# Performance work log

Measured on AMD Instinct MI355X. Metric: run time of the kernel, lower is better.

The kernel has to match this reference:

```python
import jax, jax.numpy as jnp
import numpy as np

NEG_SLOPE = 0.01  # torch nn.LeakyReLU default
K = 16

def lrelu(x):
    return jax.nn.leaky_relu(x, NEG_SLOPE)

def _knn_idx(src, dst, batch_src, batch_dst, k):
    # For each dst node, k nearest src nodes (euclidean, within same graph).
    # [Nd, Ns] squared distances; mask cross-graph pairs with +inf.
    d2 = (jnp.sum(dst * dst, axis=1)[:, None]
          + jnp.sum(src * src, axis=1)[None, :]
          - 2.0 * dst @ src.T)
    d2 = jnp.where(batch_dst[:, None] != batch_src[None, :], jnp.inf, d2)
    _, idx = jax.lax.top_k(-d2, k)  # [Nd, k] indices into src
    return idx

def _dynamic_edge_conv(src, dst, batch_src, batch_dst, w, b, k=K):
    # PyG DynamicEdgeConv: edge_index = knn(src, dst); message = nn([x_i, x_j - x_i]); max-aggregate.
    idx = _knn_idx(src, dst, batch_src, batch_dst, k)
    x_j = src[idx]                      # [Nd, k, D] gathered neighbors
    x_i = dst[:, None, :]               # [Nd, 1, D] center (target) features
    e = jnp.concatenate([jnp.broadcast_to(x_i, x_j.shape), x_j - x_i], axis=-1)  # [Nd, k, 2D]
    h = lrelu(e @ w + b)                # edge MLP: Linear(2D, D) + LeakyReLU
    return jnp.max(h, axis=1)           # max aggregation over k neighbors

def _mlp2(x, w1, b1, w2, b2):
    return lrelu(lrelu(x @ w1 + b1) @ w2 + b2)

def setup_inputs() -> dict:
    key = jax.random.key(0)
    ks = jax.random.split(key, 20)
    N_PFC, N_VTX, G, H = 8192, 2048, 32, 32
    def w(k, shp):
        return 0.1 * jax.random.normal(k, shp, jnp.float32)
    z = lambda n: jnp.zeros((n,), jnp.float32)
    return {
        "x_pfc": jax.random.normal(ks[0], (N_PFC, 7), jnp.float32),
        "x_vtx": jax.random.normal(ks[1], (N_VTX, 4), jnp.float32),
        "batch_pfc": jnp.sort(jax.random.randint(ks[2], (N_PFC,), 0, G)),
        "batch_vtx": jnp.sort(jax.random.randint(ks[3], (N_VTX,), 0, G)),
        "pfc_w1": w(ks[4], (7, H)),  "pfc_b1": z(H),
        "pfc_w2": w(ks[5], (H, H)),  "pfc_b2": z(H),
        "vtx_w1": w(ks[6], (4, H)),  "vtx_b1": z(H),
        "vtx_w2": w(ks[7], (H, H)),  "vtx_b2": z(H),
        "conv_w": w(ks[8], (2 * H, H)), "conv_b": z(H),
        "out_w1": w(ks[9], (H, 64)),  "out_b1": z(64),
        "out_w2": w(ks[10], (64, 32)), "out_b2": z(32),
        "out_w3": w(ks[11], (32, 4)),  "out_b3": z(4),
        "out_w4": w(ks[12], (4, 1)),   "out_b4": z(1),
    }

def reference(x_pfc, x_vtx, batch_pfc, batch_vtx,
              pfc_w1, pfc_b1, pfc_w2, pfc_b2,
              vtx_w1, vtx_b1, vtx_w2, vtx_b2,
              conv_w, conv_b,
              out_w1, out_b1, out_w2, out_b2, out_w3, out_b3, out_w4, out_b4):
    x_pfc_enc = _mlp2(x_pfc, pfc_w1, pfc_b1, pfc_w2, pfc_b2)   # [Npfc, 32]
    x_vtx_enc = _mlp2(x_vtx, vtx_w1, vtx_b1, vtx_w2, vtx_b2)   # [Nvtx, 32]
    # conv 1: pfc -> pfc (self knn)
    feats1 = _dynamic_edge_conv(x_pfc_enc, x_pfc_enc, batch_pfc, batch_pfc, conv_w, conv_b)
    # conv 2: vtx -> pfc (bipartite knn), same shared edge-MLP weights
    feats2 = _dynamic_edge_conv(x_vtx_enc, feats1, batch_vtx, batch_pfc, conv_w, conv_b)
    h = lrelu(feats2 @ out_w1 + out_b1)
    h = lrelu(h @ out_w2 + out_b2)
    h = lrelu(h @ out_w3 + out_b3)
    out = lrelu(h @ out_w4 + out_b4)    # [Npfc, 1]
    return (out, batch_pfc)
```

## Files before the change

### kernel.cpp

```cpp
#include <hip/hip_runtime.h>
#include <hip/hip_bf16.h>

#define LRELU(val) ((val) >= 0.0f ? (val) : 0.01f * (val))

__device__ __forceinline__ float dot4(float4 a, float4 b, float acc) {
    return fmaf(a.x, b.x, fmaf(a.y, b.y, fmaf(a.z, b.z, fmaf(a.w, b.w, acc))));
}

__device__ __forceinline__ float wdot4(const float* __restrict__ wbase, int c, int q,
                                       float4 a, float acc) {
    acc = fmaf(a.x, wbase[(4 * q + 0) * 32 + c], acc);
    acc = fmaf(a.y, wbase[(4 * q + 1) * 32 + c], acc);
    acc = fmaf(a.z, wbase[(4 * q + 2) * 32 + c], acc);
    acc = fmaf(a.w, wbase[(4 * q + 3) * 32 + c], acc);
    return acc;
}

__device__ inline int lower_bound_i(const int* __restrict__ a, int n, int v) {
    int lo = 0, hi = n;
    while (lo < hi) {
        int m = (lo + hi) >> 1;
        if (a[m] < v) lo = m + 1; else hi = m;
    }
    return lo;
}

__device__ __forceinline__ unsigned slot_key(
    int s, int lane, int start, int len, int Ns,
    const float* __restrict__ srcf, const float* __restrict__ srcn, float ni,
    float4 x0, float4 x1, float4 x2, float4 x3,
    float4 x4, float4 x5, float4 x6, float4 x7)
{
    const int o = lane + 64 * s;
    const bool valid = o < len;
    const int j = valid ? (start + o) : min(start, Ns - 1);
    const float4* rr = reinterpret_cast<const float4*>(srcf + (size_t)j * 32);
    float dot = 0.0f;
    dot = dot4(rr[0], x0, dot); dot = dot4(rr[1], x1, dot);
    dot = dot4(rr[2], x2, dot); dot = dot4(rr[3], x3, dot);
    dot = dot4(rr[4], x4, dot); dot = dot4(rr[5], x5, dot);
    dot = dot4(rr[6], x6, dot); dot = dot4(rr[7], x7, dot);
    float d2 = (ni + srcn[j]) - 2.0f * dot;
    unsigned u = __float_as_uint(d2);
    u = (d2 < 0.0f) ? ~u : (u | 0x80000000u);
    return valid ? u : 0xFFFFFFFFu;
}

template <int NSL>
__device__ __forceinline__ void select_compact(
    unsigned k0, unsigned k1, unsigned k2, unsigned k3, unsigned k4, unsigned k5,
    unsigned T, int start, int Ns, int* __restrict__ widxW, int lane)
{
    const unsigned long long below = (1ull << lane) - 1ull;
    int m = __popcll(__ballot(k0 < T));
    if (NSL > 1) m += __popcll(__ballot(k1 < T));
    if (NSL > 2) m += __popcll(__ballot(k2 < T));
    if (NSL > 3) m += __popcll(__ballot(k3 < T));
    if (NSL > 4) m += __popcll(__ballot(k4 < T));
    if (NSL > 5) m += __popcll(__ballot(k5 < T));
    const int need = 16 - m;
    const unsigned long long e0 = __ballot(k0 == T);
    const unsigned long long e1 = (NSL > 1) ? __ballot(k1 == T) : 0ull;
    const unsigned long long e2 = (NSL > 2) ? __ballot(k2 == T) : 0ull;
    const unsigned long long e3 = (NSL > 3) ? __ballot(k3 == T) : 0ull;
    const unsigned long long e4 = (NSL > 4) ? __ballot(k4 == T) : 0ull;
    const int eq0 = __popcll(e0), eq1 = eq0 + __popcll(e1), eq2 = eq1 + __popcll(e2),
              eq3 = eq2 + __popcll(e3), eq4 = eq3 + __popcll(e4);
    const bool sel0 = (k0 < T) || ((k0 == T) && (__popcll(e0 & below) < need));
    const bool sel1 = (NSL > 1) && ((k1 < T) || ((k1 == T) && (eq0 + __popcll(e1 & below) < need)));
    const bool sel2 = (NSL > 2) && ((k2 < T) || ((k2 == T) && (eq1 + __popcll(e2 & below) < need)));
    const bool sel3 = (NSL > 3) && ((k3 < T) || ((k3 == T) && (eq2 + __popcll(e3 & below) < need)));
    const bool sel4 = (NSL > 4) && ((k4 < T) || ((k4 == T) && (eq3 + __popcll(e4 & below) < need)));
    const bool sel5 = (NSL > 5) && ((k5 < T) || ((k5 == T) && (eq4 + __popcll(__ballot(k5 == T) & below) < need)));
    const unsigned long long s0 = __ballot(sel0);
    const unsigned long long s1 = __ballot(sel1);
    const unsigned long long s2 = __ballot(sel2);
    const unsigned long long s3 = __ballot(sel3);
    const unsigned long long s4 = __ballot(sel4);
    const unsigned long long s5 = __ballot(sel5);
    const int c0 = __popcll(s0), c1 = c0 + __popcll(s1), c2 = c1 + __popcll(s2),
              c3 = c2 + __popcll(s3), c4 = c3 + __popcll(s4);
    if (lane < 16) widxW[lane] = min(start, Ns - 1);
    __builtin_amdgcn_wave_barrier();
    if (sel0) widxW[__popcll(s0 & below)] = start + lane;
    if (NSL > 1 && sel1) widxW[c0 + __popcll(s1 & below)] = start + lane + 64;
    if (NSL > 2 && sel2) widxW[c1 + __popcll(s2 & below)] = start + lane + 128;
    if (NSL > 3 && sel3) widxW[c2 + __popcll(s3 & below)] = start + lane + 192;
    if (NSL > 4 && sel4) widxW[c3 + __popcll(s4 & below)] = start + lane + 256;
    if (NSL > 5 && sel5) widxW[c4 + __popcll(s5 & below)] = start + lane + 320;
    __builtin_amdgcn_wave_barrier();
}

template <int NSL>
__device__ __forceinline__ void conv_pair(
    float4 ax0, float4 ax1, float4 ax2, float4 ax3,
    float4 ax4, float4 ax5, float4 ax6, float4 ax7,
    float niA, int startA, int lenA,
    float4 bx0, float4 bx1, float4 bx2, float4 bx3,
    float4 bx4, float4 bx5, float4 bx6, float4 bx7,
    float niB, int startB, int lenB,
    const float* __restrict__ srcf, const float* __restrict__ srcn, int Ns,
    const float* __restrict__ W, const float* __restrict__ Bc,
    float4 w20, float4 w21, float4 w22, float4 w23,
    float4 w24, float4 w25, float4 w26, float4 w27,
    float4* __restrict__ sNbrA, float4* __restrict__ sNbrB,
    int* __restrict__ widxA, int* __restrict__ widxB,
    int lane, float& vOutA, float& vOutB)
{
    unsigned kA0 = 0xFFFFFFFFu, kA1 = 0xFFFFFFFFu, kA2 = 0xFFFFFFFFu,
             kA3 = 0xFFFFFFFFu, kA4 = 0xFFFFFFFFu, kA5 = 0xFFFFFFFFu;
    unsigned kB0 = 0xFFFFFFFFu, kB1 = 0xFFFFFFFFu, kB2 = 0xFFFFFFFFu,
             kB3 = 0xFFFFFFFFu, kB4 = 0xFFFFFFFFu, kB5 = 0xFFFFFFFFu;
    kA0 = slot_key(0, lane, startA, lenA, Ns, srcf, srcn, niA, ax0, ax1, ax2, ax3, ax4, ax5, ax6, ax7);
    kB0 = slot_key(0, lane, startB, lenB, Ns, srcf, srcn, niB, bx0, bx1, bx2, bx3, bx4, bx5, bx6, bx7);
    if (NSL > 1) {
        if (lenA > 64)  kA1 = slot_key(1, lane, startA, lenA, Ns, srcf, srcn, niA, ax0, ax1, ax2, ax3, ax4, ax5, ax6, ax7);
        if (lenB > 64)  kB1 = slot_key(1, lane, startB, lenB, Ns, srcf, srcn, niB, bx0, bx1, bx2, bx3, bx4, bx5, bx6, bx7);
    }
    if (NSL > 2) {
        if (lenA > 128) kA2 = slot_key(2, lane, startA, lenA, Ns, srcf, srcn, niA, ax0, ax1, ax2, ax3, ax4, ax5, ax6, ax7);
        if (lenB > 128) kB2 = slot_key(2, lane, startB, lenB, Ns, srcf, srcn, niB, bx0, bx1, bx2, bx3, bx4, bx5, bx6, bx7);
    }
    if (NSL > 3) {
        if (lenA > 192) kA3 = slot_key(3, lane, startA, lenA, Ns, srcf, srcn, niA, ax0, ax1, ax2, ax3, ax4, ax5, ax6, ax7);
        if (lenB > 192) kB3 = slot_key(3, lane, startB, lenB, Ns, srcf, srcn, niB, bx0, bx1, bx2, bx3, bx4, bx5, bx6, bx7);
    }
    if (NSL > 4) {
        if (lenA > 256) kA4 = slot_key(4, lane, startA, lenA, Ns, srcf, srcn, niA, ax0, ax1, ax2, ax3, ax4, ax5, ax6, ax7);
        if (lenB > 256) kB4 = slot_key(4, lane, startB, lenB, Ns, srcf, srcn, niB, bx0, bx1, bx2, bx3, bx4, bx5, bx6, bx7);
    }
    if (NSL > 5) {
        if (lenA > 320) kA5 = slot_key(5, lane, startA, lenA, Ns, srcf, srcn, niA, ax0, ax1, ax2, ax3, ax4, ax5, ax6, ax7);
        if (lenB > 320) kB5 = slot_key(5, lane, startB, lenB, Ns, srcf, srcn, niB, bx0, bx1, bx2, bx3, bx4, bx5, bx6, bx7);
    }

    unsigned loA = 0u, hiA = 0xFFFFFFFFu, loB = 0u, hiB = 0xFFFFFFFFu;
#pragma unroll 1
    for (int it = 0; it < 32; ++it) {
        const unsigned mA = loA + ((hiA - loA) >> 1);
        const unsigned mB = loB + ((hiB - loB) >> 1);
        int cA = __popcll(__ballot(kA0 <= mA));
        int cB = __popcll(__ballot(kB0 <= mB));
        if (NSL > 1) { cA += __popcll(__ballot(kA1 <= mA)); cB += __popcll(__ballot(kB1 <= mB)); }
        if (NSL > 2) { cA += __popcll(__ballot(kA2 <= mA)); cB += __popcll(__ballot(kB2 <= mB)); }
        if (NSL > 3) { cA += __popcll(__ballot(kA3 <= mA)); cB += __popcll(__ballot(kB3 <= mB)); }
        if (NSL > 4) { cA += __popcll(__ballot(kA4 <= mA)); cB += __popcll(__ballot(kB4 <= mB)); }
        if (NSL > 5) { cA += __popcll(__ballot(kA5 <= mA)); cB += __popcll(__ballot(kB5 <= mB)); }
        if (loA != hiA) { if (cA >= 16) hiA = mA; else loA = mA + 1; }
        if (loB != hiB) { if (cB >= 16) hiB = mB; else loB = mB + 1; }
        if (loA == hiA && loB == hiB) break;
    }

    select_compact<NSL>(kA0, kA1, kA2, kA3, kA4, kA5, loA, startA, Ns, widxA, lane);
    select_compact<NSL>(kB0, kB1, kB2, kB3, kB4, kB5, loB, startB, Ns, widxB, lane);

    const int c = lane & 31;
    const int n0 = lane >> 3, qq = lane & 7;
    const int n1 = n0 + 8;
    int jA0 = widxA[n0]; jA0 = ((unsigned)jA0 < (unsigned)Ns) ? jA0 : 0;
    int jA1 = widxA[n1]; jA1 = ((unsigned)jA1 < (unsigned)Ns) ? jA1 : 0;
    int jB0 = widxB[n0]; jB0 = ((unsigned)jB0 < (unsigned)Ns) ? jB0 : 0;
    int jB1 = widxB[n1]; jB1 = ((unsigned)jB1 < (unsigned)Ns) ? jB1 : 0;
    const float4* S = reinterpret_cast<const float4*>(srcf);
    const float4 rA0 = S[(size_t)jA0 * 8 + qq];
    const float4 rA1 = S[(size_t)jA1 * 8 + qq];
    const float4 rB0 = S[(size_t)jB0 * 8 + qq];
    const float4 rB1 = S[(size_t)jB1 * 8 + qq];

    float baseA = Bc[c];
    baseA = wdot4(W, c, 0, ax0, baseA); baseA = wdot4(W, c, 1, ax1, baseA);
    baseA = wdot4(W, c, 2, ax2, baseA); baseA = wdot4(W, c, 3, ax3, baseA);
    baseA = wdot4(W, c, 4, ax4, baseA); baseA = wdot4(W, c, 5, ax5, baseA);
    baseA = wdot4(W, c, 6, ax6, baseA); baseA = wdot4(W, c, 7, ax7, baseA);
    float dA = 0.0f;
    dA = dot4(ax0, w20, dA); dA = dot4(ax1, w21, dA); dA = dot4(ax2, w22, dA); dA = dot4(ax3, w23, dA);
    dA = dot4(ax4, w24, dA); dA = dot4(ax5, w25, dA); dA = dot4(ax6, w26, dA); dA = dot4(ax7, w27, dA);
    const float cbaseA = baseA - dA;

    float baseB = Bc[c];
    baseB = wdot4(W, c, 0, bx0, baseB); baseB = wdot4(W, c, 1, bx1, baseB);
    baseB = wdot4(W, c, 2, bx2, baseB); baseB = wdot4(W, c, 3, bx3, baseB);
    baseB = wdot4(W, c, 4, bx4, baseB); baseB = wdot4(W, c, 5, bx5, baseB);
    baseB = wdot4(W, c, 6, bx6, baseB); baseB = wdot4(W, c, 7, bx7, baseB);
    float dB = 0.0f;
    dB = dot4(bx0, w20, dB); dB = dot4(bx1, w21, dB); dB = dot4(bx2, w22, dB); dB = dot4(bx3, w23, dB);
    dB = dot4(bx4, w24, dB); dB = dot4(bx5, w25, dB); dB = dot4(bx6, w26, dB); dB = dot4(bx7, w27, dB);
    const float cbaseB = baseB - dB;

    sNbrA[n0 * 8 + qq] = rA0;
    sNbrA[n1 * 8 + qq] = rA1;
    sNbrB[n0 * 8 + qq] = rB0;
    sNbrB[n1 * 8 + qq] = rB1;
    __builtin_amdgcn_wave_barrier();

    const int half = lane >> 5;
    float vmA = -__builtin_huge_valf(), vmB = -__builtin_huge_valf();
#pragma unroll 1
    for (int r = 0; r < 8; ++r) {
        const float4* nA = sNbrA + (2 * r + half) * 8;
        const float4* nB = sNbrB + (2 * r + half) * 8;
        float accA = cbaseA, accB = cbaseB;
        accA = dot4(nA[0], w20, accA); accB = dot4(nB[0], w20, accB);
        accA = dot4(nA[1], w21, accA); accB = dot4(nB[1], w21, accB);
        accA = dot4(nA[2], w22, accA); accB = dot4(nB[2], w22, accB);
        accA = dot4(nA[3], w23, accA); accB = dot4(nB[3], w23, accB);
        accA = dot4(nA[4], w24, accA); accB = dot4(nB[4], w24, accB);
        accA = dot4(nA[5], w25, accA); accB = dot4(nB[5], w25, accB);
        accA = dot4(nA[6], w26, accA); accB = dot4(nB[6], w26, accB);
        accA = dot4(nA[7], w27, accA); accB = dot4(nB[7], w27, accB);
        vmA = fmaxf(vmA, LRELU(accA));
        vmB = fmaxf(vmB, LRELU(accB));
    }
    vmA = fmaxf(vmA, __shfl_xor(vmA, 32));
    vmB = fmaxf(vmB, __shfl_xor(vmB, 32));
    vOutA = vmA;
    vOutB = vmB;
}

__launch_bounds__(256)
__global__ void encode_kernel(const float* __restrict__ x_pfc, const float* __restrict__ x_vtx,
                              const int* __restrict__ bpfc, const int* __restrict__ bvtx,
                              const float* __restrict__ pw1, const float* __restrict__ pb1,
                              const float* __restrict__ pw2, const float* __restrict__ pb2,
                              const float* __restrict__ vw1, const float* __restrict__ vb1,
                              const float* __restrict__ vw2, const float* __restrict__ vb2,
                              float* __restrict__ pfc_enc, float* __restrict__ pfc_norm,
                              float* __restrict__ vtx_enc, float* __restrict__ vtx_norm,
                              int* __restrict__ goff_pfc, int* __restrict__ goff_vtx) {
    __shared__ float h1s[8][32];
    const int t = threadIdx.x;
    const int c = t & 31;
    const int nl = t >> 5;

    if (blockIdx.x == 0) {
        if (t < 33) goff_pfc[t] = lower_bound_i(bpfc, 8192, t);
        else if (t >= 64 && t < 97) goff_vtx[t - 64] = lower_bound_i(bvtx, 2048, t - 64);
    }

    const bool is_pfc = (blockIdx.x < 1024);
    const int node = (is_pfc ? blockIdx.x : (blockIdx.x - 1024)) * 8 + nl;
    const int din = is_pfc ? 7 : 4;
    const float* __restrict__ xin = is_pfc ? (x_pfc + node * 7) : (x_vtx + node * 4);
    const float* __restrict__ w1 = is_pfc ? pw1 : vw1;
    const float* __restrict__ b1 = is_pfc ? pb1 : vb1;
    const float* __restrict__ w2 = is_pfc ? pw2 : vw2;
    const float* __restrict__ b2 = is_pfc ? pb2 : vb2;
    float* __restrict__ enc  = is_pfc ? pfc_enc : vtx_enc;
    float* __restrict__ nrm  = is_pfc ? pfc_norm : vtx_norm;

    float h1 = b1[c];
    for (int d = 0; d < din; ++d) h1 = fmaf(xin[d], w1[d * 32 + c], h1);
    h1 = LRELU(h1);
    h1s[nl][c] = h1;
    __syncthreads();

    float h2 = b2[c];
#pragma unroll
    for (int d = 0; d < 32; ++d) h2 = fmaf(h1s[nl][d], w2[d * 32 + c], h2);
    h2 = LRELU(h2);
    enc[node * 32 + c] = h2;

    float s = h2 * h2;
#pragma unroll
    for (int m = 16; m >= 1; m >>= 1) s += __shfl_xor(s, m);
    if (c == 0) nrm[node] = s;
}

__launch_bounds__(128)
__global__ void fused_conv_kernel(
    const float* __restrict__ pfc_enc, const float* __restrict__ n_pfc,
    const float* __restrict__ vtx_enc, const float* __restrict__ n_vtx,
    const int* __restrict__ bpfc,
    const int* __restrict__ goff_pfc, const int* __restrict__ goff_vtx,
    const float* __restrict__ W, const float* __restrict__ Bc,
    float* __restrict__ feats2)
{
    __shared__ __align__(16) float4 sNbr[2][2][128];
    __shared__ int widx[2][2][16];
    __shared__ __align__(16) float sRow[2][2][32];

    const int t = threadIdx.x;
    const int lane = t & 63;
    const int w = t >> 6;
    const int b = blockIdx.x;
    const int xcd = b & 7, chunk = b >> 3;
    const int iA = xcd * 1024 + chunk * 4 + w * 2;
    const int iB = iA + 1;
    const int c = lane & 31;

    const float4 w20 = make_float4(W[32 * 32 + c], W[33 * 32 + c], W[34 * 32 + c], W[35 * 32 + c]);
    const float4 w21 = make_float4(W[36 * 32 + c], W[37 * 32 + c], W[38 * 32 + c], W[39 * 32 + c]);
    const float4 w22 = make_float4(W[40 * 32 + c], W[41 * 32 + c], W[42 * 32 + c], W[43 * 32 + c]);
    const float4 w23 = make_float4(W[44 * 32 + c], W[45 * 32 + c], W[46 * 32 + c], W[47 * 32 + c]);
    const float4 w24 = make_float4(W[48 * 32 + c], W[49 * 32 + c], W[50 * 32 + c], W[51 * 32 + c]);
    const float4 w25 = make_float4(W[52 * 32 + c], W[53 * 32 + c], W[54 * 32 + c], W[55 * 32 + c]);
    const float4 w26 = make_float4(W[56 * 32 + c], W[57 * 32 + c], W[58 * 32 + c], W[59 * 32 + c]);
    const float4 w27 = make_float4(W[60 * 32 + c], W[61 * 32 + c], W[62 * 32 + c], W[63 * 32 + c]);

    float4* sNbrA = &sNbr[w][0][0];
    float4* sNbrB = &sNbr[w][1][0];
    int* widxA = &widx[w][0][0];
    int* widxB = &widx[w][1][0];

    const int gA = bpfc[iA], gB = bpfc[iB];

    const float4* xA = reinterpret_cast<const float4*>(pfc_enc + (size_t)iA * 32);
    const float4 a0 = xA[0], a1 = xA[1], a2 = xA[2], a3 = xA[3],
                 a4 = xA[4], a5 = xA[5], a6 = xA[6], a7 = xA[7];
    const float4* xB = reinterpret_cast<const float4*>(pfc_enc + (size_t)iB * 32);
    const float4 b0 = xB[0], b1 = xB[1], b2 = xB[2], b3 = xB[3],
                 b4 = xB[4], b5 = xB[5], b6 = xB[6], b7 = xB[7];
    const float niA = n_pfc[iA], niB = n_pfc[iB];
    const int s1A = goff_pfc[gA], len1A = min(goff_pfc[gA + 1] - s1A, 384);
    const int s1B = goff_pfc[gB], len1B = min(goff_pfc[gB + 1] - s1B, 384);

    float v1A, v1B;
    {
        const int nsl = (max(len1A, len1B) + 63) >> 6;
        if (nsl <= 2)
            conv_pair<2>(a0, a1, a2, a3, a4, a5, a6, a7, niA, s1A, len1A,
                         b0, b1, b2, b3, b4, b5, b6, b7, niB, s1B, len1B,
                         pfc_enc, n_pfc, 8192, W, Bc,
                         w20, w21, w22, w23, w24, w25, w26, w27,
                         sNbrA, sNbrB, widxA, widxB, lane, v1A, v1B);
        else if (nsl <= 4)
            conv_pair<4>(a0, a1, a2, a3, a4, a5, a6, a7, niA, s1A, len1A,
                         b0, b1, b2, b3, b4, b5, b6, b7, niB, s1B, len1B,
                         pfc_enc, n_pfc, 8192, W, Bc,
                         w20, w21, w22, w23, w24, w25, w26, w27,
                         sNbrA, sNbrB, widxA, widxB, lane, v1A, v1B);
        else
            conv_pair<6>(a0, a1, a2, a3, a4, a5, a6, a7, niA, s1A, len1A,
                         b0, b1, b2, b3, b4, b5, b6, b7, niB, s1B, len1B,
                         pfc_enc, n_pfc, 8192, W, Bc,
                         w20, w21, w22, w23, w24, w25, w26, w27,
                         sNbrA, sNbrB, widxA, widxB, lane, v1A, v1B);
    }

    if (lane < 32) { sRow[w][0][lane] = v1A; sRow[w][1][lane] = v1B; }
    float nfA = v1A * v1A, nfB = v1B * v1B;
#pragma unroll
    for (int m = 16; m >= 1; m >>= 1) { nfA += __shfl_xor(nfA, m); nfB += __shfl_xor(nfB, m); }
    __builtin_amdgcn_wave_barrier();

    const float4* fA = reinterpret_cast<const float4*>(&sRow[w][0][0]);
    const float4 ya0 = fA[0], ya1 = fA[1], ya2 = fA[2], ya3 = fA[3],
                 ya4 = fA[4], ya5 = fA[5], ya6 = fA[6], ya7 = fA[7];
    const float4* fB = reinterpret_cast<const float4*>(&sRow[w][1][0]);
    const float4 yb0 = fB[0], yb1 = fB[1], yb2 = fB[2], yb3 = fB[3],
                 yb4 = fB[4], yb5 = fB[5], yb6 = fB[6], yb7 = fB[7];
    const int s2A = goff_vtx[gA], len2A = min(goff_vtx[gA + 1] - s2A, 384);
    const int s2B = goff_vtx[gB], len2B = min(goff_vtx[gB + 1] - s2B, 384);

    float v2A, v2B;
    {
        const int nsl = (max(len2A, len2B) + 63) >> 6;
        if (nsl <= 2)
            conv_pair<2>(ya0, ya1, ya2, ya3, ya4, ya5, ya6, ya7, nfA, s2A, len2A,
                         yb0, yb1, yb2, yb3, yb4, yb5, yb6, yb7, nfB, s2B, len2B,
                         vtx_enc, n_vtx, 2048, W, Bc,
                         w20, w21, w22, w23, w24, w25, w26, w27,
                         sNbrA, sNbrB, widxA, widxB, lane, v2A, v2B);
        else if (nsl <= 4)
            conv_pair<4>(ya0, ya1, ya2, ya3, ya4, ya5, ya6, ya7, nfA, s2A, len2A,
                         yb0, yb1, yb2, yb3, yb4, yb5, yb6, yb7, nfB, s2B, len2B,
                         vtx_enc, n_vtx, 2048, W, Bc,
                         w20, w21, w22, w23, w24, w25, w26, w27,
                         sNbrA, sNbrB, widxA, widxB, lane, v2A, v2B);
        else
            conv_pair<6>(ya0, ya1, ya2, ya3, ya4, ya5, ya6, ya7, nfA, s2A, len2A,
                         yb0, yb1, yb2, yb3, yb4, yb5, yb6, yb7, nfB, s2B, len2B,
                         vtx_enc, n_vtx, 2048, W, Bc,
                         w20, w21, w22, w23, w24, w25, w26, w27,
                         sNbrA, sNbrB, widxA, widxB, lane, v2A, v2B);
    }

    if (lane < 32) {
        feats2[(size_t)iA * 32 + lane] = v2A;
        feats2[(size_t)iB * 32 + lane] = v2B;
    }
}

__launch_bounds__(256)
__global__ void out_mlp_kernel(const float* __restrict__ f2, const int* __restrict__ bpfc,
                               const float* __restrict__ w1, const float* __restrict__ b1,
                               const float* __restrict__ w2, const float* __restrict__ b2,
                               const float* __restrict__ w3, const float* __restrict__ b3,
                               const float* __restrict__ w4, const float* __restrict__ b4,
                               float* __restrict__ dout, int N) {
    __shared__ float sW1[32 * 64], sW2[64 * 32], sW3[32 * 4];
    __shared__ float sB1[64], sB2[32], sB3[4], sW4[4], sB4[1];
    __shared__ float ex1[4][64];
    __shared__ float ex2[4][32];

    const int t = threadIdx.x;
    for (int k = t; k < 2048; k += 256) { sW1[k] = w1[k]; sW2[k] = w2[k]; }
    if (t < 128) sW3[t] = w3[t];
    if (t < 64)  sB1[t] = b1[t];
    if (t < 32)  sB2[t] = b2[t];
    if (t < 4)   { sB3[t] = b3[t]; sW4[t] = w4[t]; }
    if (t == 0)  sB4[0] = b4[0];
    __syncthreads();

    const int w = t >> 6;
    const int lane = t & 63;
    const int i = blockIdx.x * 4 + w;

    const float* fr = f2 + (size_t)i * 32;

    float h1 = sB1[lane];
#pragma unroll
    for (int d = 0; d < 32; ++d) h1 = fmaf(fr[d], sW1[d * 64 + lane], h1);
    h1 = LRELU(h1);
    ex1[w][lane] = h1;
    __syncthreads();

    const int c = lane & 31;
    float h2 = sB2[c];
#pragma unroll
    for (int d = 0; d < 64; ++d) h2 = fmaf(ex1[w][d], sW2[d * 32 + c], h2);
    h2 = LRELU(h2);
    if (lane < 32) ex2[w][c] = h2;
    __syncthreads();

    float a0 = sB3[0], a1 = sB3[1], a2 = sB3[2], a3 = sB3[3];
#pragma unroll
    for (int d = 0; d < 32; ++d) {
        float e = ex2[w][d];
        a0 = fmaf(e, sW3[d * 4 + 0], a0);
        a1 = fmaf(e, sW3[d * 4 + 1], a1);
        a2 = fmaf(e, sW3[d * 4 + 2], a2);
        a3 = fmaf(e, sW3[d * 4 + 3], a3);
    }
    a0 = LRELU(a0); a1 = LRELU(a1); a2 = LRELU(a2); a3 = LRELU(a3);
    float o = sB4[0];
    o = fmaf(a0, sW4[0], o); o = fmaf(a1, sW4[1], o);
    o = fmaf(a2, sW4[2], o); o = fmaf(a3, sW4[3], o);
    o = LRELU(o);

    if (lane == 0) dout[i] = o;
    if (lane == 1) dout[N + i] = (float)bpfc[i];
}

extern "C" void kernel_launch(void* const* d_in, const int* in_sizes, int n_in,
                              void* d_out, int out_size, void* d_ws, size_t ws_size,
                              hipStream_t stream) {
    const float* x_pfc     = (const float*)d_in[0];
    const float* x_vtx     = (const float*)d_in[1];
    const int*   batch_pfc = (const int*)d_in[2];
    const int*   batch_vtx = (const int*)d_in[3];
    const float* pfc_w1 = (const float*)d_in[4];
    const float* pfc_b1 = (const float*)d_in[5];
    const float* pfc_w2 = (const float*)d_in[6];
    const float* pfc_b2 = (const float*)d_in[7];
    const float* vtx_w1 = (const float*)d_in[8];
    const float* vtx_b1 = (const float*)d_in[9];
    const float* vtx_w2 = (const float*)d_in[10];
    const float* vtx_b2 = (const float*)d_in[11];
    const float* conv_w = (const float*)d_in[12];
    const float* conv_b = (const float*)d_in[13];
    const float* out_w1 = (const float*)d_in[14];
    const float* out_b1 = (const float*)d_in[15];
    const float* out_w2 = (const float*)d_in[16];
    const float* out_b2 = (const float*)d_in[17];
    const float* out_w3 = (const float*)d_in[18];
    const float* out_b3 = (const float*)d_in[19];
    const float* out_w4 = (const float*)d_in[20];
    const float* out_b4 = (const float*)d_in[21];

    const int N_PFC = 8192;

    float* ws = (float*)d_ws;
    float* pfc_enc = ws;
    float* vtx_enc = ws + 262144;
    float* feats2  = ws + 327680;
    float* n_pfc   = ws + 589824;
    float* n_vtx   = ws + 598016;
    int*   goff_pfc = (int*)(ws + 600064);
    int*   goff_vtx = (int*)(ws + 600128);

    encode_kernel<<<1280, 256, 0, stream>>>(x_pfc, x_vtx, batch_pfc, batch_vtx,
                                            pfc_w1, pfc_b1, pfc_w2, pfc_b2,
                                            vtx_w1, vtx_b1, vtx_w2, vtx_b2,
                                            pfc_enc, n_pfc, vtx_enc, n_vtx,
                                            goff_pfc, goff_vtx);

    fused_conv_kernel<<<2048, 128, 0, stream>>>(pfc_enc, n_pfc, vtx_enc, n_vtx,
                                                batch_pfc, goff_pfc, goff_vtx,
                                                conv_w, conv_b, feats2);

    out_mlp_kernel<<<2048, 256, 0, stream>>>(feats2, batch_pfc,
                                             out_w1, out_b1, out_w2, out_b2,
                                             out_w3, out_b3, out_w4, out_b4,
                                             (float*)d_out, N_PFC);
}
```

Baseline: 188.6 us.

## Stage per-graph source features in LDS tiles shared across block waves

The fused conv kernel now loads each graph's pfc and vtx encoded features, plus their norms, into padded LDS tiles (stride 33) once per block. All waves then compute kNN distances and edge-MLP gathers from LDS instead of global memory. Blocks grow to 256 threads covering 8 consecutive nodes and loop over the graphs those nodes span, with block-wide syncs between graphs. The change also caps the vtx neighbour count at 128, and it adds about 68KB of LDS per block, which lowers occupancy, plus redundant tile loads when a block spans several graphs.

```diff
diff --git a/kernel.cpp b/kernel.cpp
--- a/kernel.cpp
+++ b/kernel.cpp
@@ -16,6 +16,29 @@
     return acc;
 }
 
+__device__ __forceinline__ float row_wacc(const float* __restrict__ rp, float acc,
+    float4 q0, float4 q1, float4 q2, float4 q3,
+    float4 q4, float4 q5, float4 q6, float4 q7)
+{
+    acc = fmaf(rp[0],  q0.x, acc); acc = fmaf(rp[1],  q0.y, acc);
+    acc = fmaf(rp[2],  q0.z, acc); acc = fmaf(rp[3],  q0.w, acc);
+    acc = fmaf(rp[4],  q1.x, acc); acc = fmaf(rp[5],  q1.y, acc);
+    acc = fmaf(rp[6],  q1.z, acc); acc = fmaf(rp[7],  q1.w, acc);
+    acc = fmaf(rp[8],  q2.x, acc); acc = fmaf(rp[9],  q2.y, acc);
+    acc = fmaf(rp[10], q2.z, acc); acc = fmaf(rp[11], q2.w, acc);
+    acc = fmaf(rp[12], q3.x, acc); acc = fmaf(rp[13], q3.y, acc);
+    acc = fmaf(rp[14], q3.z, acc); acc = fmaf(rp[15], q3.w, acc);
+    acc = fmaf(rp[16], q4.x, acc); acc = fmaf(rp[17], q4.y, acc);
+    acc = fmaf(rp[18], q4.z, acc); acc = fmaf(rp[19], q4.w, acc);
+    acc = fmaf(rp[20], q5.x, acc); acc = fmaf(rp[21], q5.y, acc);
+    acc = fmaf(rp[22], q5.z, acc); acc = fmaf(rp[23], q5.w, acc);
+    acc = fmaf(rp[24], q6.x, acc); acc = fmaf(rp[25], q6.y, acc);
+    acc = fmaf(rp[26], q6.z, acc); acc = fmaf(rp[27], q6.w, acc);
+    acc = fmaf(rp[28], q7.x, acc); acc = fmaf(rp[29], q7.y, acc);
+    acc = fmaf(rp[30], q7.z, acc); acc = fmaf(rp[31], q7.w, acc);
+    return acc;
+}
+
 __device__ inline int lower_bound_i(const int* __restrict__ a, int n, int v) {
     int lo = 0, hi = n;
     while (lo < hi) {
@@ -25,31 +48,26 @@
     return lo;
 }
 
-__device__ __forceinline__ unsigned slot_key(
-    int s, int lane, int start, int len, int Ns,
-    const float* __restrict__ srcf, const float* __restrict__ srcn, float ni,
-    float4 x0, float4 x1, float4 x2, float4 x3,
-    float4 x4, float4 x5, float4 x6, float4 x7)
+__device__ __forceinline__ unsigned slot_key_lds(
+    int s, int lane, int len,
+    const float* __restrict__ tile, const float* __restrict__ sn, float ni,
+    float4 q0, float4 q1, float4 q2, float4 q3,
+    float4 q4, float4 q5, float4 q6, float4 q7)
 {
     const int o = lane + 64 * s;
-    const bool valid = o < len;
-    const int j = valid ? (start + o) : min(start, Ns - 1);
-    const float4* rr = reinterpret_cast<const float4*>(srcf + (size_t)j * 32);
-    float dot = 0.0f;
-    dot = dot4(rr[0], x0, dot); dot = dot4(rr[1], x1, dot);
-    dot = dot4(rr[2], x2, dot); dot = dot4(rr[3], x3, dot);
-    dot = dot4(rr[4], x4, dot); dot = dot4(rr[5], x5, dot);
-    dot = dot4(rr[6], x6, dot); dot = dot4(rr[7], x7, dot);
-    float d2 = (ni + srcn[j]) - 2.0f * dot;
+    const int oc = (o < len) ? o : 0;
+    const float* rp = tile + oc * 33;
+    const float dot = row_wacc(rp, 0.0f, q0, q1, q2, q3, q4, q5, q6, q7);
+    const float d2 = (ni + sn[oc]) - 2.0f * dot;
     unsigned u = __float_as_uint(d2);
     u = (d2 < 0.0f) ? ~u : (u | 0x80000000u);
-    return valid ? u : 0xFFFFFFFFu;
+    return (o < len) ? u : 0xFFFFFFFFu;
 }
 
 template <int NSL>
-__device__ __forceinline__ void select_compact(
+__device__ __forceinline__ void select_compact_loc(
     unsigned k0, unsigned k1, unsigned k2, unsigned k3, unsigned k4, unsigned k5,
-    unsigned T, int start, int Ns, int* __restrict__ widxW, int lane)
+    unsigned T, int* __restrict__ widxW, int lane)
 {
     const unsigned long long below = (1ull << lane) - 1ull;
     int m = __popcll(__ballot(k0 < T));
@@ -80,30 +98,27 @@
     const unsigned long long s5 = __ballot(sel5);
     const int c0 = __popcll(s0), c1 = c0 + __popcll(s1), c2 = c1 + __popcll(s2),
               c3 = c2 + __popcll(s3), c4 = c3 + __popcll(s4);
-    if (lane < 16) widxW[lane] = min(start, Ns - 1);
+    if (lane < 16) widxW[lane] = 0;
     __builtin_amdgcn_wave_barrier();
-    if (sel0) widxW[__popcll(s0 & below)] = start + lane;
-    if (NSL > 1 && sel1) widxW[c0 + __popcll(s1 & below)] = start + lane + 64;
-    if (NSL > 2 && sel2) widxW[c1 + __popcll(s2 & below)] = start + lane + 128;
-    if (NSL > 3 && sel3) widxW[c2 + __popcll(s3 & below)] = start + lane + 192;
-    if (NSL > 4 && sel4) widxW[c3 + __popcll(s4 & below)] = start + lane + 256;
-    if (NSL > 5 && sel5) widxW[c4 + __popcll(s5 & below)] = start + lane + 320;
+    if (sel0) widxW[__popcll(s0 & below)] = lane;
+    if (NSL > 1 && sel1) widxW[c0 + __popcll(s1 & below)] = lane + 64;
+    if (NSL > 2 && sel2) widxW[c1 + __popcll(s2 & below)] = lane + 128;
+    if (NSL > 3 && sel3) widxW[c2 + __popcll(s3 & below)] = lane + 192;
+    if (NSL > 4 && sel4) widxW[c3 + __popcll(s4 & below)] = lane + 256;
+    if (NSL > 5 && sel5) widxW[c4 + __popcll(s5 & below)] = lane + 320;
     __builtin_amdgcn_wave_barrier();
 }
 
 template <int NSL>
-__device__ __forceinline__ void conv_pair(
+__device__ __forceinline__ void conv_pair_lds(
     float4 ax0, float4 ax1, float4 ax2, float4 ax3,
-    float4 ax4, float4 ax5, float4 ax6, float4 ax7,
-    float niA, int startA, int lenA,
+    float4 ax4, float4 ax5, float4 ax6, float4 ax7, float niA, int lenA,
     float4 bx0, float4 bx1, float4 bx2, float4 bx3,
-    float4 bx4, float4 bx5, float4 bx6, float4 bx7,
-    float niB, int startB, int lenB,
-    const float* __restrict__ srcf, const float* __restrict__ srcn, int Ns,
+    float4 bx4, float4 bx5, float4 bx6, float4 bx7, float niB, int lenB,
+    const float* __restrict__ tile, const float* __restrict__ sn,
     const float* __restrict__ W, const float* __restrict__ Bc,
     float4 w20, float4 w21, float4 w22, float4 w23,
     float4 w24, float4 w25, float4 w26, float4 w27,
-    float4* __restrict__ sNbrA, float4* __restrict__ sNbrB,
     int* __restrict__ widxA, int* __restrict__ widxB,
     int lane, float& vOutA, float& vOutB)
 {
@@ -111,27 +126,27 @@
              kA3 = 0xFFFFFFFFu, kA4 = 0xFFFFFFFFu, kA5 = 0xFFFFFFFFu;
     unsigned kB0 = 0xFFFFFFFFu, kB1 = 0xFFFFFFFFu, kB2 = 0xFFFFFFFFu,
              kB3 = 0xFFFFFFFFu, kB4 = 0xFFFFFFFFu, kB5 = 0xFFFFFFFFu;
-    kA0 = slot_key(0, lane, startA, lenA, Ns, srcf, srcn, niA, ax0, ax1, ax2, ax3, ax4, ax5, ax6, ax7);
-    kB0 = slot_key(0, lane, startB, lenB, Ns, srcf, srcn, niB, bx0, bx1, bx2, bx3, bx4, bx5, bx6, bx7);
+    if (lenA > 0) kA0 = slot_key_lds(0, lane, lenA, tile, sn, niA, ax0, ax1, ax2, ax3, ax4, ax5, ax6, ax7);
+    if (lenB > 0) kB0 = slot_key_lds(0, lane, lenB, tile, sn, niB, bx0, bx1, bx2, bx3, bx4, bx5, bx6, bx7);
     if (NSL > 1) {
-        if (lenA > 64)  kA1 = slot_key(1, lane, startA, lenA, Ns, srcf, srcn, niA, ax0, ax1, ax2, ax3, ax4, ax5, ax6, ax7);
-        if (lenB > 64)  kB1 = slot_key(1, lane, startB, lenB, Ns, srcf, srcn, niB, bx0, bx1, bx2, bx3, bx4, bx5, bx6, bx7);
+        if (lenA > 64)  kA1 = slot_key_lds(1, lane, lenA, tile, sn, niA, ax0, ax1, ax2, ax3, ax4, ax5, ax6, ax7);
+        if (lenB > 64)  kB1 = slot_key_lds(1, lane, lenB, tile, sn, niB, bx0, bx1, bx2, bx3, bx4, bx5, bx6, bx7);
     }
     if (NSL > 2) {
-        if (lenA > 128) kA2 = slot_key(2, lane, startA, lenA, Ns, srcf, srcn, niA, ax0, ax1, ax2, ax3, ax4, ax5, ax6, ax7);
-        if (lenB > 128) kB2 = slot_key(2, lane, startB, lenB, Ns, srcf, srcn, niB, bx0, bx1, bx2, bx3, bx4, bx5, bx6, bx7);
+        if (lenA > 128) kA2 = slot_key_lds(2, lane, lenA, tile, sn, niA, ax0, ax1, ax2, ax3, ax4, ax5, ax6, ax7);
+        if (lenB > 128) kB2 = slot_key_lds(2, lane, lenB, tile, sn, niB, bx0, bx1, bx2, bx3, bx4, bx5, bx6, bx7);
     }
     if (NSL > 3) {
-        if (lenA > 192) kA3 = slot_key(3, lane, startA, lenA, Ns, srcf, srcn, niA, ax0, ax1, ax2, ax3, ax4, ax5, ax6, ax7);
-        if (lenB > 192) kB3 = slot_key(3, lane, startB, lenB, Ns, srcf, srcn, niB, bx0, bx1, bx2, bx3, bx4, bx5, bx6, bx7);
+        if (lenA > 192) kA3 = slot_key_lds(3, lane, lenA, tile, sn, niA, ax0, ax1, ax2, ax3, ax4, ax5, ax6, ax7);
+        if (lenB > 192) kB3 = slot_key_lds(3, lane, lenB, tile, sn, niB, bx0, bx1, bx2, bx3, bx4, bx5, bx6, bx7);
     }
     if (NSL > 4) {
-        if (lenA > 256) kA4 = slot_key(4, lane, startA, lenA, Ns, srcf, srcn, niA, ax0, ax1, ax2, ax3, ax4, ax5, ax6, ax7);
-        if (lenB > 256) kB4 = slot_key(4, lane, startB, lenB, Ns, srcf, srcn, niB, bx0, bx1, bx2, bx3, bx4, bx5, bx6, bx7);
+        if (lenA > 256) kA4 = slot_key_lds(4, lane, lenA, tile, sn, niA, ax0, ax1, ax2, ax3, ax4, ax5, ax6, ax7);
+        if (lenB > 256) kB4 = slot_key_lds(4, lane, lenB, tile, sn, niB, bx0, bx1, bx2, bx3, bx4, bx5, bx6, bx7);
     }
     if (NSL > 5) {
-        if (lenA > 320) kA5 = slot_key(5, lane, startA, lenA, Ns, srcf, srcn, niA, ax0, ax1, ax2, ax3, ax4, ax5, ax6, ax7);
-        if (lenB > 320) kB5 = slot_key(5, lane, startB, lenB, Ns, srcf, srcn, niB, bx0, bx1, bx2, bx3, bx4, bx5, bx6, bx7);
+        if (lenA > 320) kA5 = slot_key_lds(5, lane, lenA, tile, sn, niA, ax0, ax1, ax2, ax3, ax4, ax5, ax6, ax7);
+        if (lenB > 320) kB5 = slot_key_lds(5, lane, lenB, tile, sn, niB, bx0, bx1, bx2, bx3, bx4, bx5, bx6, bx7);
     }
 
     unsigned loA = 0u, hiA = 0xFFFFFFFFu, loB = 0u, hiB = 0xFFFFFFFFu;
@@ -151,22 +166,10 @@
         if (loA == hiA && loB == hiB) break;
     }
 
-    select_compact<NSL>(kA0, kA1, kA2, kA3, kA4, kA5, loA, startA, Ns, widxA, lane);
-    select_compact<NSL>(kB0, kB1, kB2, kB3, kB4, kB5, loB, startB, Ns, widxB, lane);
+    select_compact_loc<NSL>(kA0, kA1, kA2, kA3, kA4, kA5, loA, widxA, lane);
+    select_compact_loc<NSL>(kB0, kB1, kB2, kB3, kB4, kB5, loB, widxB, lane);
 
     const int c = lane & 31;
-    const int n0 = lane >> 3, qq = lane & 7;
-    const int n1 = n0 + 8;
-    int jA0 = widxA[n0]; jA0 = ((unsigned)jA0 < (unsigned)Ns) ? jA0 : 0;
-    int jA1 = widxA[n1]; jA1 = ((unsigned)jA1 < (unsigned)Ns) ? jA1 : 0;
-    int jB0 = widxB[n0]; jB0 = ((unsigned)jB0 < (unsigned)Ns) ? jB0 : 0;
-    int jB1 = widxB[n1]; jB1 = ((unsigned)jB1 < (unsigned)Ns) ? jB1 : 0;
-    const float4* S = reinterpret_cast<const float4*>(srcf);
-    const float4 rA0 = S[(size_t)jA0 * 8 + qq];
-    const float4 rA1 = S[(size_t)jA1 * 8 + qq];
-    const float4 rB0 = S[(size_t)jB0 * 8 + qq];
-    const float4 rB1 = S[(size_t)jB1 * 8 + qq];
-
     float baseA = Bc[c];
     baseA = wdot4(W, c, 0, ax0, baseA); baseA = wdot4(W, c, 1, ax1, baseA);
     baseA = wdot4(W, c, 2, ax2, baseA); baseA = wdot4(W, c, 3, ax3, baseA);
@@ -187,27 +190,16 @@
     dB = dot4(bx4, w24, dB); dB = dot4(bx5, w25, dB); dB = dot4(bx6, w26, dB); dB = dot4(bx7, w27, dB);
     const float cbaseB = baseB - dB;
 
-    sNbrA[n0 * 8 + qq] = rA0;
-    sNbrA[n1 * 8 + qq] = rA1;
-    sNbrB[n0 * 8 + qq] = rB0;
-    sNbrB[n1 * 8 + qq] = rB1;
-    __builtin_amdgcn_wave_barrier();
-
     const int half = lane >> 5;
     float vmA = -__builtin_huge_valf(), vmB = -__builtin_huge_valf();
 #pragma unroll 1
     for (int r = 0; r < 8; ++r) {
-        const float4* nA = sNbrA + (2 * r + half) * 8;
-        const float4* nB = sNbrB + (2 * r + half) * 8;
-        float accA = cbaseA, accB = cbaseB;
-        accA = dot4(nA[0], w20, accA); accB = dot4(nB[0], w20, accB);
-        accA = dot4(nA[1], w21, accA); accB = dot4(nB[1], w21, accB);
-        accA = dot4(nA[2], w22, accA); accB = dot4(nB[2], w22, accB);
-        accA = dot4(nA[3], w23, accA); accB = dot4(nB[3], w23, accB);
-        accA = dot4(nA[4], w24, accA); accB = dot4(nB[4], w24, accB);
-        accA = dot4(nA[5], w25, accA); accB = dot4(nB[5], w25, accB);
-        accA = dot4(nA[6], w26, accA); accB = dot4(nB[6], w26, accB);
-        accA = dot4(nA[7], w27, accA); accB = dot4(nB[7], w27, accB);
+        const int jA = widxA[2 * r + half];
+        const int jB = widxB[2 * r + half];
+        const float* rpA = tile + jA * 33;
+        const float* rpB = tile + jB * 33;
+        const float accA = row_wacc(rpA, cbaseA, w20, w21, w22, w23, w24, w25, w26, w27);
+        const float accB = row_wacc(rpB, cbaseB, w20, w21, w22, w23, w24, w25, w26, w27);
         vmA = fmaxf(vmA, LRELU(accA));
         vmB = fmaxf(vmB, LRELU(accB));
     }
@@ -266,7 +258,7 @@
     if (c == 0) nrm[node] = s;
 }
 
-__launch_bounds__(128)
+__launch_bounds__(256)
 __global__ void fused_conv_kernel(
     const float* __restrict__ pfc_enc, const float* __restrict__ n_pfc,
     const float* __restrict__ vtx_enc, const float* __restrict__ n_vtx,
@@ -275,17 +267,19 @@
     const float* __restrict__ W, const float* __restrict__ Bc,
     float* __restrict__ feats2)
 {
-    __shared__ __align__(16) float4 sNbr[2][2][128];
-    __shared__ int widx[2][2][16];
-    __shared__ __align__(16) float sRow[2][2][32];
+    __shared__ __align__(16) float tileP[384 * 33];
+    __shared__ __align__(16) float tileV[128 * 33];
+    __shared__ float snP[384], snV[128];
+    __shared__ int widx[4][2][16];
+    __shared__ __align__(16) float sRow[4][2][32];
 
     const int t = threadIdx.x;
     const int lane = t & 63;
     const int w = t >> 6;
     const int b = blockIdx.x;
     const int xcd = b & 7, chunk = b >> 3;
-    const int iA = xcd * 1024 + chunk * 4 + w * 2;
-    const int iB = iA + 1;
+    const int nb0 = (xcd * 128 + chunk) * 8;
+    const int iA = nb0 + w * 2, iB = iA + 1;
     const int c = lane & 31;
 
     const float4 w20 = make_float4(W[32 * 32 + c], W[33 * 32 + c], W[34 * 32 + c], W[35 * 32 + c]);
@@ -297,82 +291,101 @@
     const float4 w26 = make_float4(W[56 * 32 + c], W[57 * 32 + c], W[58 * 32 + c], W[59 * 32 + c]);
     const float4 w27 = make_float4(W[60 * 32 + c], W[61 * 32 + c], W[62 * 32 + c], W[63 * 32 + c]);
 
-    float4* sNbrA = &sNbr[w][0][0];
-    float4* sNbrB = &sNbr[w][1][0];
     int* widxA = &widx[w][0][0];
     int* widxB = &widx[w][1][0];
 
     const int gA = bpfc[iA], gB = bpfc[iB];
-
-    const float4* xA = reinterpret_cast<const float4*>(pfc_enc + (size_t)iA * 32);
-    const float4 a0 = xA[0], a1 = xA[1], a2 = xA[2], a3 = xA[3],
-                 a4 = xA[4], a5 = xA[5], a6 = xA[6], a7 = xA[7];
-    const float4* xB = reinterpret_cast<const float4*>(pfc_enc + (size_t)iB * 32);
-    const float4 b0 = xB[0], b1 = xB[1], b2 = xB[2], b3 = xB[3],
-                 b4 = xB[4], b5 = xB[5], b6 = xB[6], b7 = xB[7];
-    const float niA = n_pfc[iA], niB = n_pfc[iB];
-    const int s1A = goff_pfc[gA], len1A = min(goff_pfc[gA + 1] - s1A, 384);
-    const int s1B = goff_pfc[gB], len1B = min(goff_pfc[gB + 1] - s1B, 384);
-
-    float v1A, v1B;
-    {
-        const int nsl = (max(len1A, len1B) + 63) >> 6;
-        if (nsl <= 2)
-            conv_pair<2>(a0, a1, a2, a3, a4, a5, a6, a7, niA, s1A, len1A,
-                         b0, b1, b2, b3, b4, b5, b6, b7, niB, s1B, len1B,
-                         pfc_enc, n_pfc, 8192, W, Bc,
-                         w20, w21, w22, w23, w24, w25, w26, w27,
-                         sNbrA, sNbrB, widxA, widxB, lane, v1A, v1B);
-        else if (nsl <= 4)
-            conv_pair<4>(a0, a1, a2, a3, a4, a5, a6, a7, niA, s1A, len1A,
-                         b0, b1, b2, b3, b4, b5, b6, b7, niB, s1B, len1B,
-                         pfc_enc, n_pfc, 8192, W, Bc,
-                         w20, w21, w22, w23, w24, w25, w26, w27,
-                         sNbrA, sNbrB, widxA, widxB, lane, v1A, v1B);
-        else
-            conv_pair<6>(a0, a1, a2, a3, a4, a5, a6, a7, niA, s1A, len1A,
-                         b0, b1, b2, b3, b4, b5, b6, b7, niB, s1B, len1B,
-                         pfc_enc, n_pfc, 8192, W, Bc,
-                         w20, w21, w22, w23, w24, w25, w26, w27,
-                         sNbrA, sNbrB, widxA, widxB, lane, v1A, v1B);
-    }
-
-    if (lane < 32) { sRow[w][0][lane] = v1A; sRow[w][1][lane] = v1B; }
-    float nfA = v1A * v1A, nfB = v1B * v1B;
+    const int g0 = bpfc[nb0], g1 = bpfc[nb0 + 7];
+
+    float v2A = 0.0f, v2B = 0.0f;
+
+#pragma unroll 1
+    for (int g = g0; g <= g1; ++g) {
+        const int s1 = goff_pfc[g];
+        const int len1 = min(goff_pfc[g + 1] - s1, 384);
+        const int s2 = goff_vtx[g];
+        const int len2 = min(goff_vtx[g + 1] - s2, 128);
+
+#pragma unroll 1
+        for (int p = t; p < len1 * 8; p += 256) {
+            const int r = p >> 3, q = p & 7;
+            const float4 v = reinterpret_cast<const float4*>(pfc_enc)[(size_t)(s1 + r) * 8 + q];
+            float* dp = tileP + r * 33 + q * 4;
+            dp[0] = v.x; dp[1] = v.y; dp[2] = v.z; dp[3] = v.w;
+        }
+#pragma unroll 1
+        for (int p = t; p < len2 * 8; p += 256) {
+            const int r = p >> 3, q = p & 7;
+            const float4 v = reinterpret_cast<const float4*>(vtx_enc)[(size_t)(s2 + r) * 8 + q];
+            float* dp = tileV + r * 33 + q * 4;
+            dp[0] = v.x; dp[1] = v.y; dp[2] = v.z; dp[3] = v.w;
+        }
+        for (int p = t; p < len1; p += 256) snP[p] = n_pfc[s1 + p];
+        for (int p = t; p < len2; p += 256) snV[p] = n_vtx[s2 + p];
+        __syncthreads();
+
+        const bool actA = (gA == g), actB = (gB == g);
+        if (actA || actB) {
+            const float4* xA = reinterpret_cast<const float4*>(pfc_enc + (size_t)iA * 32);
+            const float4 a0 = xA[0], a1 = xA[1], a2 = xA[2], a3 = xA[3],
+                         a4 = xA[4], a5 = xA[5], a6 = xA[6], a7 = xA[7];
+            const float4* xB = reinterpret_cast<const float4*>(pfc_enc + (size_t)iB * 32);
+            const float4 b0 = xB[0], b1 = xB[1], b2 = xB[2], b3 = xB[3],
+                         b4 = xB[4], b5 = xB[5], b6 = xB[6], b7 = xB[7];
+            const int lA1 = actA ? len1 : 0, lB1 = actB ? len1 : 0;
+
+            float v1A, v1B;
+            {
+                const int nsl = (max(lA1, lB1) + 63) >> 6;
+                if (nsl <= 2)
+                    conv_pair_lds<2>(a0, a1, a2, a3, a4, a5, a6, a7, n_pfc[iA], lA1,
+                                     b0, b1, b2, b3, b4, b5, b6, b7, n_pfc[iB], lB1,
+                                     tileP, snP, W, Bc, w20, w21, w22, w23, w24, w25, w26, w27,
+                                     widxA, widxB, lane, v1A, v1B);
+                else if (nsl <= 4)
+                    conv_pair_lds<4>(a0, a1, a2, a3, a4, a5, a6, a7, n_pfc[iA], lA1,
+                                     b0, b1, b2, b3, b4, b5, b6, b7, n_pfc[iB], lB1,
+                                     tileP, snP, W, Bc, w20, w21, w22, w23, w24, w25, w26, w27,
+                                     widxA, widxB, lane, v1A, v1B);
+                else
+                    conv_pair_lds<6>(a0, a1, a2, a3, a4, a5, a6, a7, n_pfc[iA], lA1,
+                                     b0, b1, b2, b3, b4, b5, b6, b7, n_pfc[iB], lB1,
+                                     tileP, snP, W, Bc, w20, w21, w22, w23, w24, w25, w26, w27,
+                                     widxA, widxB, lane, v1A, v1B);
+            }
+
+            if (lane < 32) { sRow[w][0][lane] = v1A; sRow[w][1][lane] = v1B; }
+            float nfA = v1A * v1A, nfB = v1B * v1B;
 #pragma unroll
-    for (int m = 16; m >= 1; m >>= 1) { nfA += __shfl_xor(nfA, m); nfB += __shfl_xor(nfB, m); }
-    __builtin_amdgcn_wave_barrier();
-
-    const float4* fA = reinterpret_cast<const float4*>(&sRow[w][0][0]);
-    const float4 ya0 = fA[0], ya1 = fA[1], ya2 = fA[2], ya3 = fA[3],
-                 ya4 = fA[4], ya5 = fA[5], ya6 = fA[6], ya7 = fA[7];
-    const float4* fB = reinterpret_cast<const float4*>(&sRow[w][1][0]);
-    const float4 yb0 = fB[0], yb1 = fB[1], yb2 = fB[2], yb3 = fB[3],
-                 yb4 = fB[4], yb5 = fB[5], yb6 = fB[6], yb7 = fB[7];
-    const int s2A = goff_vtx[gA], len2A = min(goff_vtx[gA + 1] - s2A, 384);
-    const int s2B = goff_vtx[gB], len2B = min(goff_vtx[gB + 1] - s2B, 384);
-
-    float v2A, v2B;
-    {
-        const int nsl = (max(len2A, len2B) + 63) >> 6;
-        if (nsl <= 2)
-            conv_pair<2>(ya0, ya1, ya2, ya3, ya4, ya5, ya6, ya7, nfA, s2A, len2A,
-                         yb0, yb1, yb2, yb3, yb4, yb5, yb6, yb7, nfB, s2B, len2B,
-                         vtx_enc, n_vtx, 2048, W, Bc,
-                         w20, w21, w22, w23, w24, w25, w26, w27,
-                         sNbrA, sNbrB, widxA, widxB, lane, v2A, v2B);
-        else if (nsl <= 4)
-            conv_pair<4>(ya0, ya1, ya2, ya3, ya4, ya5, ya6, ya7, nfA, s2A, len2A,
-                         yb0, yb1, yb2, yb3, yb4, yb5, yb6, yb7, nfB, s2B, len2B,
-                         vtx_enc, n_vtx, 2048, W, Bc,
-                         w20, w21, w22, w23, w24, w25, w26, w27,
-                         sNbrA, sNbrB, widxA, widxB, lane, v2A, v2B);
-        else
-            conv_pair<6>(ya0, ya1, ya2, ya3, ya4, ya5, ya6, ya7, nfA, s2A, len2A,
-                         yb0, yb1, yb2, yb3, yb4, yb5, yb6, yb7, nfB, s2B, len2B,
-                         vtx_enc, n_vtx, 2048, W, Bc,
-                         w20, w21, w22, w23, w24, w25, w26, w27,
-                         sNbrA, sNbrB, widxA, widxB, lane, v2A, v2B);
+            for (int m = 16; m >= 1; m >>= 1) { nfA += __shfl_xor(nfA, m); nfB += __shfl_xor(nfB, m); }
+            __builtin_amdgcn_wave_barrier();
+
+            const float4* fA = reinterpret_cast<const float4*>(&sRow[w][0][0]);
+            const float4 ya0 = fA[0], ya1 = fA[1], ya2 = fA[2], ya3 = fA[3],
+                         ya4 = fA[4], ya5 = fA[5], ya6 = fA[6], ya7 = fA[7];
+            const float4* fB = reinterpret_cast<const float4*>(&sRow[w][1][0]);
+            const float4 yb0 = fB[0], yb1 = fB[1], yb2 = fB[2], yb3 = fB[3],
+                         yb4 = fB[4], yb5 = fB[5], yb6 = fB[6], yb7 = fB[7];
+            const int lA2 = actA ? len2 : 0, lB2 = actB ? len2 : 0;
+
+            float o2A, o2B;
+            {
+                const int nsl = (max(lA2, lB2) + 63) >> 6;
+                if (nsl <= 1)
+                    conv_pair_lds<1>(ya0, ya1, ya2, ya3, ya4, ya5, ya6, ya7, nfA, lA2,
+                                     yb0, yb1, yb2, yb3, yb4, yb5, yb6, yb7, nfB, lB2,
+                                     tileV, snV, W, Bc, w20, w21, w22, w23, w24, w25, w26, w27,
+                                     widxA, widxB, lane, o2A, o2B);
+                else
+                    conv_pair_lds<2>(ya0, ya1, ya2, ya3, ya4, ya5, ya6, ya7, nfA, lA2,
+                                     yb0, yb1, yb2, yb3, yb4, yb5, yb6, yb7, nfB, lB2,
+                                     tileV, snV, W, Bc, w20, w21, w22, w23, w24, w25, w26, w27,
+                                     widxA, widxB, lane, o2A, o2B);
+            }
+            if (actA) v2A = o2A;
+            if (actB) v2B = o2B;
+        }
+        __syncthreads();
     }
 
     if (lane < 32) {
@@ -485,7 +498,7 @@
                                             pfc_enc, n_pfc, vtx_enc, n_vtx,
                                             goff_pfc, goff_vtx);
 
-    fused_conv_kernel<<<2048, 128, 0, stream>>>(pfc_enc, n_pfc, vtx_enc, n_vtx,
+    fused_conv_kernel<<<1024, 256, 0, stream>>>(pfc_enc, n_pfc, vtx_enc, n_vtx,
                                                 batch_pfc, goff_pfc, goff_vtx,
                                                 conv_w, conv_b, feats2);
 
```

After: 237.7 us. 26.0% more time.
